# Optimization experiments

Hardware: AMD Instinct MI355X
Metric: run time of the kernel (lower is better)

## Reference

```python
import jax, jax.numpy as jnp
import numpy as np

HEAD_DIM = 64
NUM_HEAD = 12
NUM_LANDMARKS = 64
SEQ_LEN = 4096
BATCH = 8
NEG_BIG = 1e9


def setup_inputs() -> dict:
    key = jax.random.key(0)
    k1, k2, k3 = jax.random.split(key, 3)
    shape = (BATCH, NUM_HEAD, SEQ_LEN, HEAD_DIM)
    Q = jax.random.normal(k1, shape, dtype=jnp.float32)
    K = jax.random.normal(k2, shape, dtype=jnp.float32)
    V = jax.random.normal(k3, shape, dtype=jnp.float32)
    mask = jnp.ones((BATCH, SEQ_LEN), dtype=jnp.float32)
    return {"Q": Q, "K": K, "V": V, "mask": mask}


def iterative_inv(mat, n_iter=6):
    # Newton-Schulz iteration for Moore-Penrose pseudo-inverse ('original' init)
    I = jnp.eye(mat.shape[-1], dtype=mat.dtype)
    Km = mat
    Vi = Km.swapaxes(-1, -2) / jnp.max(jnp.sum(Km, axis=-2))
    for _ in range(n_iter):
        KV = Km @ Vi  # [B,H,L,L]
        Vi = 0.25 * Vi @ (13.0 * I - KV @ (15.0 * I - KV @ (7.0 * I - KV)))
    return Vi


def reference(Q, K, V, mask):
    scale = 1.0 / np.sqrt(np.sqrt(HEAD_DIM))  # divide by d^(1/4) on both Q and K
    m = mask[:, None, :, None]
    Qs = Q * m * scale
    Ks = K * m * scale

    B = Qs.shape[0]
    seg = SEQ_LEN // NUM_LANDMARKS
    # landmarks: segment means over the sequence -> [B,H,L,D]
    Q_l = Qs.reshape(B, NUM_HEAD, NUM_LANDMARKS, seg, HEAD_DIM).mean(axis=-2)
    K_l = Ks.reshape(B, NUM_HEAD, NUM_LANDMARKS, seg, HEAD_DIM).mean(axis=-2)

    # kernel_1: [B,H,S,L], kernel_2: [B,H,L,L], kernel_3: [B,H,L,S]
    kernel_1 = jax.nn.softmax(jnp.einsum('bhsd,bhld->bhsl', Qs, K_l), axis=-1)
    kernel_2 = jax.nn.softmax(jnp.einsum('bhld,bhmd->bhlm', Q_l, K_l), axis=-1)
    kernel_3 = jax.nn.softmax(
        jnp.einsum('bhld,bhsd->bhls', Q_l, Ks) - NEG_BIG * (1.0 - mask[:, None, None, :]),
        axis=-1)

    X = (kernel_1 @ iterative_inv(kernel_2)) @ (kernel_3 @ V)  # [B,H,S,D]
    return X
```

## Files before the change

kernel.cpp:

```cpp
#include <hip/hip_runtime.h>
#include <stdint.h>

#define BATCH 8
#define NH 12
#define SL 4096
#define HD 64
#define NL 64
#define SEG 64
#define BHN (BATCH*NH)
#define SCALE 0.35355339059327373f
#define LP 68

typedef unsigned short bfu;
typedef __attribute__((ext_vector_type(8))) short bhalf8;
typedef __attribute__((ext_vector_type(4))) float floatx4;

__device__ __forceinline__ float bf2f(bfu u) { return __uint_as_float(((unsigned)u) << 16); }
__device__ __forceinline__ bfu f2bf(float f) {
    unsigned u = __float_as_uint(f);
    u += 0x7fffu + ((u >> 16) & 1u);
    return (bfu)(u >> 16);
}
__device__ __forceinline__ void split(float x, bfu& h, bfu& l) {
    h = f2bf(x);
    l = f2bf(x - bf2f(h));
}
__device__ __forceinline__ unsigned pack2(bfu a, bfu b) { return (unsigned)a | ((unsigned)b << 16); }

__device__ __forceinline__ float ld1(const void* p, size_t i, int f32) {
    return f32 ? ((const float*)p)[i] : bf2f(((const bfu*)p)[i]);
}
__device__ __forceinline__ void ld4(const void* p, size_t i, int f32, float o[4]) {
    if (f32) {
        float4 v = *(const float4*)((const float*)p + i);
        o[0] = v.x; o[1] = v.y; o[2] = v.z; o[3] = v.w;
    } else {
        ushort4 v = *(const ushort4*)((const bfu*)p + i);
        o[0] = bf2f(v.x); o[1] = bf2f(v.y); o[2] = bf2f(v.z); o[3] = bf2f(v.w);
    }
}

template<int PA, int PB>
__device__ __forceinline__ void mm64(const float* A, const float* B, float acc[4][4], int tr, int tc) {
#pragma unroll
    for (int k4 = 0; k4 < 16; ++k4) {
        alignas(16) float a[4][4];
#pragma unroll
        for (int i = 0; i < 4; ++i)
            *(float4*)(&a[i][0]) = *(const float4*)(A + (4*tr + i)*PA + 4*k4);
#pragma unroll
        for (int kk = 0; kk < 4; ++kk) {
            float4 b = *(const float4*)(B + (4*k4 + kk)*PB + 4*tc);
#pragma unroll
            for (int i = 0; i < 4; ++i) {
                acc[i][0] = fmaf(a[i][kk], b.x, acc[i][0]);
                acc[i][1] = fmaf(a[i][kk], b.y, acc[i][1]);
                acc[i][2] = fmaf(a[i][kk], b.z, acc[i][2]);
                acc[i][3] = fmaf(a[i][kk], b.w, acc[i][3]);
            }
        }
    }
}

__device__ __forceinline__ bhalf8 ldfrag(const bfu* S, int row, int kb) {
    const uint2 a = *(const uint2*)(S + row*LP + kb);
    const uint2 b = *(const uint2*)(S + row*LP + kb + 16);
    union { uint4 u; bhalf8 s; } cv;
    cv.u.x = a.x; cv.u.y = a.y; cv.u.z = b.x; cv.u.w = b.y;
    return cv.s;
}

__device__ __forceinline__ void mfma64(const bfu* Ah, const bfu* Am,
                                       const bfu* Bh, const bfu* Bl,
                                       int w, int l, floatx4 acc[4]) {
    const int r15 = l & 15, kg = (l >> 4) << 2;
    bhalf8 ah[2], al[2];
    ah[0] = ldfrag(Ah, 16*w + r15, kg);
    ah[1] = ldfrag(Ah, 16*w + r15, 32 + kg);
    al[0] = ldfrag(Am, 16*w + r15, kg);
    al[1] = ldfrag(Am, 16*w + r15, 32 + kg);
#pragma unroll
    for (int t = 0; t < 4; ++t) {
#pragma unroll
        for (int c = 0; c < 2; ++c) {
            bhalf8 bh = ldfrag(Bh, 16*t + r15, 32*c + kg);
            bhalf8 bl = ldfrag(Bl, 16*t + r15, 32*c + kg);
            acc[t] = __builtin_amdgcn_mfma_f32_16x16x32_bf16(ah[c], bh, acc[t], 0, 0, 0);
            acc[t] = __builtin_amdgcn_mfma_f32_16x16x32_bf16(ah[c], bl, acc[t], 0, 0, 0);
            acc[t] = __builtin_amdgcn_mfma_f32_16x16x32_bf16(al[c], bh, acc[t], 0, 0, 0);
        }
    }
}

__global__ void detect_k(const void* __restrict__ M, int* __restrict__ dflag) {
    if (threadIdx.x == 0) {
        unsigned v = *(const unsigned*)M;
        dflag[0] = (v == 0x3F800000u) ? 1 : 0;
    }
}

__global__ __launch_bounds__(64) void landmarks_k(const void* __restrict__ Q, const void* __restrict__ K,
                                                  const void* __restrict__ M, const int* __restrict__ dt,
                                                  float* __restrict__ Ql, float* __restrict__ Kl) {
    int f32 = dt[0];
    int bh = blockIdx.x, l = blockIdx.y, d = threadIdx.x;
    int b = bh / NH;
    size_t qb = ((size_t)(bh*SL) + l*SEG)*HD + d;
    size_t mb = (size_t)b*SL + l*SEG;
    float aq = 0.f, ak = 0.f;
#pragma unroll 8
    for (int i = 0; i < SEG; ++i) {
        float mk = ld1(M, mb + i, f32);
        aq += ld1(Q, qb + (size_t)i*HD, f32) * mk;
        ak += ld1(K, qb + (size_t)i*HD, f32) * mk;
    }
    float sc = SCALE / (float)SEG;
    Ql[(bh*NL + l)*HD + d] = aq * sc;
    Kl[(bh*NL + l)*HD + d] = ak * sc;
}

__global__ __launch_bounds__(256) void k2_kernel(const float* __restrict__ Ql, const float* __restrict__ Kl,
                                                 float* __restrict__ K2, float* __restrict__ cmax) {
    __shared__ float Qs[64*68];
    __shared__ float Bs[64*68];
    __shared__ float Cs[64*68];
    int bh = blockIdx.x, t = threadIdx.x;
    int tr = t >> 4, tc = t & 15;
    for (int idx = t; idx < 4096; idx += 256) {
        int r = idx >> 6, c = idx & 63;
        Qs[r*68 + c] = Ql[(bh*64 + r)*64 + c];
        Bs[c*68 + r] = Kl[(bh*64 + r)*64 + c];
    }
    __syncthreads();
    float acc[4][4] = {};
    mm64<68,68>(Qs, Bs, acc, tr, tc);
#pragma unroll
    for (int i = 0; i < 4; ++i)
        *(float4*)&Cs[(4*tr + i)*68 + 4*tc] = make_float4(acc[i][0], acc[i][1], acc[i][2], acc[i][3]);
    __syncthreads();
    if (t < 64) {
        float mx = -1e30f;
        for (int m = 0; m < 64; ++m) mx = fmaxf(mx, Cs[t*68 + m]);
        float s = 0.f;
        for (int m = 0; m < 64; ++m) { float e = __expf(Cs[t*68 + m] - mx); Cs[t*68 + m] = e; s += e; }
        float r = 1.f / s;
        for (int m = 0; m < 64; ++m) Cs[t*68 + m] *= r;
    }
    __syncthreads();
    for (int idx = t; idx < 4096; idx += 256) {
        int r = idx >> 6, c = idx & 63;
        K2[bh*4096 + idx] = Cs[r*68 + c];
    }
    if (t < 64) {
        float cs = 0.f;
        for (int l = 0; l < 64; ++l) cs += Cs[l*68 + t];
        for (int off = 32; off > 0; off >>= 1) cs = fmaxf(cs, __shfl_xor(cs, off, 64));
        if (t == 0) cmax[bh] = cs;
    }
}

template<int NC>
__global__ __launch_bounds__(256) void k3v_partial(const void* __restrict__ K, const void* __restrict__ V,
                                                   const void* __restrict__ M, const int* __restrict__ dt,
                                                   const float* __restrict__ Ql,
                                                   float* __restrict__ Opart, float* __restrict__ mpart,
                                                   float* __restrict__ lpart) {
    __shared__ bfu Qh[64*LP], Qm[64*LP];
    __shared__ bfu Bh[64*LP], Bl[64*LP];
    __shared__ bfu Ph[64*LP], Pl[64*LP];
    __shared__ float bias[64];
    int f32 = dt[0];
    int bh = blockIdx.x, ch = blockIdx.y, b = bh / NH;
    int t = threadIdx.x, w = t >> 6, l = t & 63, r15 = l & 15;

    for (int g = t; g < 1024; g += 256) {
        int rr = g >> 4, c4 = (g & 15) << 2;
        float4 v = *(const float4*)(Ql + (bh*64 + rr)*64 + c4);
        bfu h0,h1,h2,h3,l0,l1,l2,l3;
        split(v.x,h0,l0); split(v.y,h1,l1); split(v.z,h2,l2); split(v.w,h3,l3);
        *(uint2*)&Qh[rr*LP + c4] = make_uint2(pack2(h0,h1), pack2(h2,h3));
        *(uint2*)&Qm[rr*LP + c4] = make_uint2(pack2(l0,l1), pack2(l2,l3));
    }
    floatx4 accO[4];
#pragma unroll
    for (int i = 0; i < 4; ++i) accO[i] = (floatx4){0.f,0.f,0.f,0.f};
    float mrow[4] = {-1e38f,-1e38f,-1e38f,-1e38f};
    float lrow[4] = {0.f,0.f,0.f,0.f};
    const int chunkN = SL / NC;
    int s0 = ch * chunkN;

    for (int st = 0; st < chunkN/64; ++st) {
        int sbase = s0 + st*64;
        __syncthreads();
        for (int g = t; g < 1024; g += 256) {
            int j = g >> 4, d4 = (g & 15) << 2;
            float v[4];
            ld4(K, ((size_t)(bh*SL) + sbase + j)*HD + d4, f32, v);
            float mk = ld1(M, (size_t)b*SL + sbase + j, f32) * SCALE;
            bfu h0,h1,h2,h3,l0,l1,l2,l3;
            split(v[0]*mk,h0,l0); split(v[1]*mk,h1,l1); split(v[2]*mk,h2,l2); split(v[3]*mk,h3,l3);
            *(uint2*)&Bh[j*LP + d4] = make_uint2(pack2(h0,h1), pack2(h2,h3));
            *(uint2*)&Bl[j*LP + d4] = make_uint2(pack2(l0,l1), pack2(l2,l3));
        }
        if (t < 64) bias[t] = -1000000000.0f * (1.f - ld1(M, (size_t)b*SL + sbase + t, f32));
        __syncthreads();
        floatx4 accS[4];
#pragma unroll
        for (int i = 0; i < 4; ++i) accS[i] = (floatx4){0.f,0.f,0.f,0.f};
        mfma64(Qh, Qm, Bh, Bl, w, l, accS);
#pragma unroll
        for (int t4 = 0; t4 < 4; ++t4) {
            float bc = bias[16*t4 + r15];
#pragma unroll
            for (int r = 0; r < 4; ++r) accS[t4][r] += bc;
        }
#pragma unroll
        for (int r = 0; r < 4; ++r) {
            float mx = fmaxf(fmaxf(accS[0][r], accS[1][r]), fmaxf(accS[2][r], accS[3][r]));
            mx = fmaxf(mx, __shfl_xor(mx, 1, 64));
            mx = fmaxf(mx, __shfl_xor(mx, 2, 64));
            mx = fmaxf(mx, __shfl_xor(mx, 4, 64));
            mx = fmaxf(mx, __shfl_xor(mx, 8, 64));
            float mnew = fmaxf(mrow[r], mx);
            float al = __expf(mrow[r] - mnew);
            float s = 0.f;
#pragma unroll
            for (int t4 = 0; t4 < 4; ++t4) {
                float e = __expf(accS[t4][r] - mnew);
                accS[t4][r] = e;
                s += e;
            }
            s += __shfl_xor(s, 1, 64);
            s += __shfl_xor(s, 2, 64);
            s += __shfl_xor(s, 4, 64);
            s += __shfl_xor(s, 8, 64);
            lrow[r] = lrow[r]*al + s;
            mrow[r] = mnew;
#pragma unroll
            for (int t4 = 0; t4 < 4; ++t4) accO[t4][r] *= al;
        }
#pragma unroll
        for (int t4 = 0; t4 < 4; ++t4)
#pragma unroll
            for (int r = 0; r < 4; ++r) {
                int row = 16*w + ((l>>4)<<2) + r, col = 16*t4 + r15;
                bfu h, lo;
                split(accS[t4][r], h, lo);
                Ph[row*LP + col] = h;
                Pl[row*LP + col] = lo;
            }
        __syncthreads();
        {
            int d = t & 63, j4g = t >> 6;
            for (int j4 = j4g; j4 < 16; j4 += 4) {
                float v0 = ld1(V, ((size_t)(bh*SL) + sbase + 4*j4 + 0)*HD + d, f32);
                float v1 = ld1(V, ((size_t)(bh*SL) + sbase + 4*j4 + 1)*HD + d, f32);
                float v2 = ld1(V, ((size_t)(bh*SL) + sbase + 4*j4 + 2)*HD + d, f32);
                float v3 = ld1(V, ((size_t)(bh*SL) + sbase + 4*j4 + 3)*HD + d, f32);
                bfu h0,h1,h2,h3,l0,l1,l2,l3;
                split(v0,h0,l0); split(v1,h1,l1); split(v2,h2,l2); split(v3,h3,l3);
                *(uint2*)&Bh[d*LP + 4*j4] = make_uint2(pack2(h0,h1), pack2(h2,h3));
                *(uint2*)&Bl[d*LP + 4*j4] = make_uint2(pack2(l0,l1), pack2(l2,l3));
            }
        }
        __syncthreads();
        mfma64(Ph, Pl, Bh, Bl, w, l, accO);
    }
    __syncthreads();
    int pc = bh*NC + ch;
    if (r15 == 0) {
#pragma unroll
        for (int r = 0; r < 4; ++r) {
            int row = 16*w + ((l>>4)<<2) + r;
            mpart[pc*64 + row] = mrow[r];
            lpart[pc*64 + row] = lrow[r];
        }
    }
#pragma unroll
    for (int t4 = 0; t4 < 4; ++t4)
#pragma unroll
        for (int r = 0; r < 4; ++r) {
            int row = 16*w + ((l>>4)<<2) + r, col = 16*t4 + r15;
            Opart[(size_t)pc*4096 + row*64 + col] = accO[t4][r];
        }
}

template<int NC>
__global__ __launch_bounds__(256) void combine_k(const float* __restrict__ Opart, const float* __restrict__ mpart,
                                                 const float* __restrict__ lpart, float* __restrict__ K3V) {
    __shared__ float coef[NC][64];
    int bh = blockIdx.x, t = threadIdx.x;
    if (t < 64) {
        float mg = -1e38f;
        for (int ch = 0; ch < NC; ++ch) mg = fmaxf(mg, mpart[(bh*NC + ch)*64 + t]);
        float e[NC];
        float sg = 0.f;
        for (int ch = 0; ch < NC; ++ch) {
            e[ch] = __expf(mpart[(bh*NC + ch)*64 + t] - mg);
            sg += e[ch] * lpart[(bh*NC + ch)*64 + t];
        }
        float r = 1.f / fmaxf(sg, 1e-37f);
        for (int ch = 0; ch < NC; ++ch) coef[ch][t] = e[ch] * r;
    }
    __syncthreads();
    int c = t & 63, lq = t >> 6;
    for (int k = 0; k < 16; ++k) {
        int l = 4*k + lq;
        float s = 0.f;
#pragma unroll
        for (int ch = 0; ch < NC; ++ch)
            s += coef[ch][l] * Opart[(size_t)(bh*NC + ch)*4096 + l*64 + c];
        K3V[(bh*64 + l)*64 + c] = s;
    }
}

__global__ __launch_bounds__(256) void inv_kernel(const float* __restrict__ K2, const float* __restrict__ cmaxArr,
                                                  const float* __restrict__ K3V, float* __restrict__ WT) {
    __shared__ float Km[4096];
    __shared__ float Vi[4096];
    __shared__ float B1[4096];
    __shared__ float B2[4096];
    int bh = blockIdx.x, t = threadIdx.x, tr = t >> 4, tc = t & 15;
    float cm = 0.f;
    for (int i = 0; i < BHN; ++i) cm = fmaxf(cm, cmaxArr[i]);
    float rc = 1.f / fmaxf(cm, 1e-37f);
    for (int idx = t; idx < 4096; idx += 256) Km[idx] = K2[bh*4096 + idx];
    __syncthreads();
    for (int idx = t; idx < 4096; idx += 256) {
        int i = idx >> 6, j = idx & 63;
        Vi[idx] = Km[j*64 + i] * rc;
    }
    __syncthreads();
    float acc[4][4];
    for (int it = 0; it < 6; ++it) {
#pragma unroll
        for (int i = 0; i < 4; ++i) for (int j = 0; j < 4; ++j) acc[i][j] = 0.f;
        mm64<64,64>(Km, Vi, acc, tr, tc);
#pragma unroll
        for (int i = 0; i < 4; ++i)
            *(float4*)&B1[(4*tr + i)*64 + 4*tc] = make_float4(acc[i][0], acc[i][1], acc[i][2], acc[i][3]);
        __syncthreads();
#pragma unroll
        for (int i = 0; i < 4; ++i) for (int j = 0; j < 4; ++j) acc[i][j] = 0.f;
        mm64<64,64>(B1, B1, acc, tr, tc);
#pragma unroll
        for (int i = 0; i < 4; ++i)
#pragma unroll
            for (int j = 0; j < 4; ++j) acc[i][j] = 7.f*B1[(4*tr + i)*64 + 4*tc + j] - acc[i][j];
#pragma unroll
        for (int i = 0; i < 4; ++i)
            *(float4*)&B2[(4*tr + i)*64 + 4*tc] = make_float4(acc[i][0], acc[i][1], acc[i][2], acc[i][3]);
        __syncthreads();
#pragma unroll
        for (int i = 0; i < 4; ++i) for (int j = 0; j < 4; ++j) acc[i][j] = 0.f;
        mm64<64,64>(B1, B2, acc, tr, tc);
#pragma unroll
        for (int i = 0; i < 4; ++i)
#pragma unroll
            for (int j = 0; j < 4; ++j) acc[i][j] = 15.f*B1[(4*tr + i)*64 + 4*tc + j] - acc[i][j];
        __syncthreads();
#pragma unroll
        for (int i = 0; i < 4; ++i)
            *(float4*)&B2[(4*tr + i)*64 + 4*tc] = make_float4(acc[i][0], acc[i][1], acc[i][2], acc[i][3]);
        __syncthreads();
#pragma unroll
        for (int i = 0; i < 4; ++i) for (int j = 0; j < 4; ++j) acc[i][j] = 0.f;
        mm64<64,64>(Vi, B2, acc, tr, tc);
        __syncthreads();
#pragma unroll
        for (int i = 0; i < 4; ++i)
#pragma unroll
            for (int j = 0; j < 4; ++j) {
                int off = (4*tr + i)*64 + 4*tc + j;
                Vi[off] = 3.25f*Vi[off] - 0.25f*acc[i][j];
            }
        __syncthreads();
    }
    for (int idx = t; idx < 4096; idx += 256) B1[idx] = K3V[bh*4096 + idx];
    __syncthreads();
#pragma unroll
    for (int i = 0; i < 4; ++i) for (int j = 0; j < 4; ++j) acc[i][j] = 0.f;
    mm64<64,64>(Vi, B1, acc, tr, tc);
#pragma unroll
    for (int i = 0; i < 4; ++i)
#pragma unroll
        for (int j = 0; j < 4; ++j)
            WT[(size_t)bh*4096 + (4*tc + j)*64 + (4*tr + i)] = acc[i][j];
}

__global__ __launch_bounds__(256) void final_k(const void* __restrict__ Q, const void* __restrict__ M,
                                               const int* __restrict__ dt,
                                               const float* __restrict__ Kl, const float* __restrict__ WT,
                                               void* __restrict__ X) {
    __shared__ bfu Ah[64*LP], Am[64*LP];
    __shared__ bfu Kh[64*LP], Km2[64*LP];
    __shared__ bfu Wh[64*LP], Wl[64*LP];
    int f32 = dt[0];
    int bh = blockIdx.x, tile = blockIdx.y, b = bh / NH;
    int t = threadIdx.x, w = t >> 6, l = t & 63, r15 = l & 15;
    int s0 = tile * 64;
    for (int g = t; g < 1024; g += 256) {
        int rr = g >> 4, d4 = (g & 15) << 2;
        float v[4];
        ld4(Q, ((size_t)(bh*SL) + s0 + rr)*HD + d4, f32, v);
        float mk = ld1(M, (size_t)b*SL + s0 + rr, f32) * SCALE;
        bfu h0,h1,h2,h3,l0,l1,l2,l3;
        split(v[0]*mk,h0,l0); split(v[1]*mk,h1,l1); split(v[2]*mk,h2,l2); split(v[3]*mk,h3,l3);
        *(uint2*)&Ah[rr*LP + d4] = make_uint2(pack2(h0,h1), pack2(h2,h3));
        *(uint2*)&Am[rr*LP + d4] = make_uint2(pack2(l0,l1), pack2(l2,l3));
    }
    for (int g = t; g < 1024; g += 256) {
        int rr = g >> 4, c4 = (g & 15) << 2;
        float4 v1 = *(const float4*)(Kl + bh*4096 + rr*64 + c4);
        bfu h0,h1,h2,h3,l0,l1,l2,l3;
        split(v1.x,h0,l0); split(v1.y,h1,l1); split(v1.z,h2,l2); split(v1.w,h3,l3);
        *(uint2*)&Kh[rr*LP + c4]  = make_uint2(pack2(h0,h1), pack2(h2,h3));
        *(uint2*)&Km2[rr*LP + c4] = make_uint2(pack2(l0,l1), pack2(l2,l3));
        float4 v2 = *(const float4*)(WT + (size_t)bh*4096 + rr*64 + c4);
        split(v2.x,h0,l0); split(v2.y,h1,l1); split(v2.z,h2,l2); split(v2.w,h3,l3);
        *(uint2*)&Wh[rr*LP + c4] = make_uint2(pack2(h0,h1), pack2(h2,h3));
        *(uint2*)&Wl[rr*LP + c4] = make_uint2(pack2(l0,l1), pack2(l2,l3));
    }
    __syncthreads();
    floatx4 accS[4];
#pragma unroll
    for (int i = 0; i < 4; ++i) accS[i] = (floatx4){0.f,0.f,0.f,0.f};
    mfma64(Ah, Am, Kh, Km2, w, l, accS);
#pragma unroll
    for (int r = 0; r < 4; ++r) {
        float mx = fmaxf(fmaxf(accS[0][r], accS[1][r]), fmaxf(accS[2][r], accS[3][r]));
        mx = fmaxf(mx, __shfl_xor(mx, 1, 64));
        mx = fmaxf(mx, __shfl_xor(mx, 2, 64));
        mx = fmaxf(mx, __shfl_xor(mx, 4, 64));
        mx = fmaxf(mx, __shfl_xor(mx, 8, 64));
        float s = 0.f;
#pragma unroll
        for (int t4 = 0; t4 < 4; ++t4) {
            float e = __expf(accS[t4][r] - mx);
            accS[t4][r] = e;
            s += e;
        }
        s += __shfl_xor(s, 1, 64);
        s += __shfl_xor(s, 2, 64);
        s += __shfl_xor(s, 4, 64);
        s += __shfl_xor(s, 8, 64);
        float inv = 1.f / s;
#pragma unroll
        for (int t4 = 0; t4 < 4; ++t4) accS[t4][r] *= inv;
    }
    __syncthreads();
#pragma unroll
    for (int t4 = 0; t4 < 4; ++t4)
#pragma unroll
        for (int r = 0; r < 4; ++r) {
            int row = 16*w + ((l>>4)<<2) + r, col = 16*t4 + r15;
            bfu h, lo;
            split(accS[t4][r], h, lo);
            Ah[row*LP + col] = h;
            Am[row*LP + col] = lo;
        }
    __syncthreads();
    floatx4 accO[4];
#pragma unroll
    for (int i = 0; i < 4; ++i) accO[i] = (floatx4){0.f,0.f,0.f,0.f};
    mfma64(Ah, Am, Wh, Wl, w, l, accO);
#pragma unroll
    for (int t4 = 0; t4 < 4; ++t4)
#pragma unroll
        for (int r = 0; r < 4; ++r) {
            int row = 16*w + ((l>>4)<<2) + r, col = 16*t4 + r15;
            size_t base = ((size_t)(bh*SL) + s0 + row)*HD + col;
            if (f32) ((float*)X)[base] = accO[t4][r];
            else     ((bfu*)X)[base] = f2bf(accO[t4][r]);
        }
}

extern "C" void kernel_launch(void* const* d_in, const int* in_sizes, int n_in,
                              void* d_out, int out_size, void* d_ws, size_t ws_size,
                              hipStream_t stream) {
    const void* Q = d_in[0];
    const void* K = d_in[1];
    const void* V = d_in[2];
    const void* M = d_in[3];
    float* ws = (float*)d_ws;

    auto layout_bytes = [](int nc) -> size_t {
        size_t o = 64 + 5*(size_t)BHN*4096 + 2*(size_t)BHN*nc*64 + 128 + (size_t)BHN*nc*4096;
        return o * 4;
    };
    int NC = (ws_size >= layout_bytes(8)) ? 8 : 4;

    size_t o = 0;
    int*   dflag = (int*)(ws + o); o += 64;
    float* Ql    = ws + o; o += (size_t)BHN*64*64;
    float* Kl    = ws + o; o += (size_t)BHN*64*64;
    float* K2    = ws + o; o += (size_t)BHN*64*64;
    float* K3V   = ws + o; o += (size_t)BHN*64*64;
    float* WT    = ws + o; o += (size_t)BHN*64*64;
    float* mpart = ws + o; o += (size_t)BHN*NC*64;
    float* lpart = ws + o; o += (size_t)BHN*NC*64;
    float* cmax  = ws + o; o += 128;
    float* Opart = ws + o; o += (size_t)BHN*NC*64*64;

    detect_k<<<1, 64, 0, stream>>>(M, dflag);
    landmarks_k<<<dim3(BHN, NL), 64, 0, stream>>>(Q, K, M, dflag, Ql, Kl);
    k2_kernel<<<BHN, 256, 0, stream>>>(Ql, Kl, K2, cmax);
    if (NC == 8) {
        k3v_partial<8><<<dim3(BHN, 8), 256, 0, stream>>>(K, V, M, dflag, Ql, Opart, mpart, lpart);
        combine_k<8><<<BHN, 256, 0, stream>>>(Opart, mpart, lpart, K3V);
    } else {
        k3v_partial<4><<<dim3(BHN, 4), 256, 0, stream>>>(K, V, M, dflag, Ql, Opart, mpart, lpart);
        combine_k<4><<<BHN, 256, 0, stream>>>(Opart, mpart, lpart, K3V);
    }
    inv_kernel<<<BHN, 256, 0, stream>>>(K2, cmax, K3V, WT);
    final_k<<<dim3(BHN, SL/64), 256, 0, stream>>>(Q, M, dflag, Kl, WT, d_out);
}
```

Measured before the change: 530.1 us.

## Pre-split landmarks and W into bf16 hi/lo pairs; process two tiles per final block

Landmark Q/K and the inverse-weight matrix are now split into bf16 hi/lo pairs once, in their producer kernels, and stored that way in global memory. Consumers (k2, k3v_partial, final_k) load the pairs directly instead of re-splitting fp32 values in every block. final_k now handles two 64-row sequence tiles per block, so the K-landmark and W staging into shared memory is amortised over twice the work and the grid is halved. The trade-off is fewer blocks in final_k for latency hiding, plus an extra sync per tile iteration.

```diff
diff --git a/kernel.cpp b/kernel.cpp
--- a/kernel.cpp
+++ b/kernel.cpp
@@ -101,7 +101,8 @@
 
 __global__ __launch_bounds__(64) void landmarks_k(const void* __restrict__ Q, const void* __restrict__ K,
                                                   const void* __restrict__ M, const int* __restrict__ dt,
-                                                  float* __restrict__ Ql, float* __restrict__ Kl) {
+                                                  bfu* __restrict__ Qlh, bfu* __restrict__ Qll,
+                                                  bfu* __restrict__ Klh, bfu* __restrict__ Kll) {
     int f32 = dt[0];
     int bh = blockIdx.x, l = blockIdx.y, d = threadIdx.x;
     int b = bh / NH;
@@ -115,11 +116,17 @@
         ak += ld1(K, qb + (size_t)i*HD, f32) * mk;
     }
     float sc = SCALE / (float)SEG;
-    Ql[(bh*NL + l)*HD + d] = aq * sc;
-    Kl[(bh*NL + l)*HD + d] = ak * sc;
-}
-
-__global__ __launch_bounds__(256) void k2_kernel(const float* __restrict__ Ql, const float* __restrict__ Kl,
+    float qv = aq * sc, kv = ak * sc;
+    bfu qh, ql_, kh, kl_;
+    split(qv, qh, ql_);
+    split(kv, kh, kl_);
+    size_t gi = (size_t)(bh*NL + l)*HD + d;
+    Qlh[gi] = qh; Qll[gi] = ql_;
+    Klh[gi] = kh; Kll[gi] = kl_;
+}
+
+__global__ __launch_bounds__(256) void k2_kernel(const bfu* __restrict__ Qlh, const bfu* __restrict__ Qll,
+                                                 const bfu* __restrict__ Klh, const bfu* __restrict__ Kll,
                                                  float* __restrict__ K2, float* __restrict__ cmax) {
     __shared__ float Qs[64*68];
     __shared__ float Bs[64*68];
@@ -128,8 +135,9 @@
     int tr = t >> 4, tc = t & 15;
     for (int idx = t; idx < 4096; idx += 256) {
         int r = idx >> 6, c = idx & 63;
-        Qs[r*68 + c] = Ql[(bh*64 + r)*64 + c];
-        Bs[c*68 + r] = Kl[(bh*64 + r)*64 + c];
+        size_t gi = (size_t)bh*4096 + idx;
+        Qs[r*68 + c] = bf2f(Qlh[gi]) + bf2f(Qll[gi]);
+        Bs[c*68 + r] = bf2f(Klh[gi]) + bf2f(Kll[gi]);
     }
     __syncthreads();
     float acc[4][4] = {};
@@ -162,7 +170,7 @@
 template<int NC>
 __global__ __launch_bounds__(256) void k3v_partial(const void* __restrict__ K, const void* __restrict__ V,
                                                    const void* __restrict__ M, const int* __restrict__ dt,
-                                                   const float* __restrict__ Ql,
+                                                   const bfu* __restrict__ Qlh, const bfu* __restrict__ Qll,
                                                    float* __restrict__ Opart, float* __restrict__ mpart,
                                                    float* __restrict__ lpart) {
     __shared__ bfu Qh[64*LP], Qm[64*LP];
@@ -175,11 +183,9 @@
 
     for (int g = t; g < 1024; g += 256) {
         int rr = g >> 4, c4 = (g & 15) << 2;
-        float4 v = *(const float4*)(Ql + (bh*64 + rr)*64 + c4);
-        bfu h0,h1,h2,h3,l0,l1,l2,l3;
-        split(v.x,h0,l0); split(v.y,h1,l1); split(v.z,h2,l2); split(v.w,h3,l3);
-        *(uint2*)&Qh[rr*LP + c4] = make_uint2(pack2(h0,h1), pack2(h2,h3));
-        *(uint2*)&Qm[rr*LP + c4] = make_uint2(pack2(l0,l1), pack2(l2,l3));
+        size_t gi = (size_t)bh*4096 + rr*64 + c4;
+        *(uint2*)&Qh[rr*LP + c4] = *(const uint2*)(Qlh + gi);
+        *(uint2*)&Qm[rr*LP + c4] = *(const uint2*)(Qll + gi);
     }
     floatx4 accO[4];
 #pragma unroll
@@ -315,7 +321,8 @@
 }
 
 __global__ __launch_bounds__(256) void inv_kernel(const float* __restrict__ K2, const float* __restrict__ cmaxArr,
-                                                  const float* __restrict__ K3V, float* __restrict__ WT) {
+                                                  const float* __restrict__ K3V,
+                                                  bfu* __restrict__ WTh, bfu* __restrict__ WTl) {
     __shared__ float Km[4096];
     __shared__ float Vi[4096];
     __shared__ float B1[4096];
@@ -384,95 +391,103 @@
 #pragma unroll
     for (int i = 0; i < 4; ++i)
 #pragma unroll
-        for (int j = 0; j < 4; ++j)
-            WT[(size_t)bh*4096 + (4*tc + j)*64 + (4*tr + i)] = acc[i][j];
+        for (int j = 0; j < 4; ++j) {
+            bfu h, lo;
+            split(acc[i][j], h, lo);
+            size_t gi = (size_t)bh*4096 + (4*tc + j)*64 + (4*tr + i);
+            WTh[gi] = h;
+            WTl[gi] = lo;
+        }
 }
 
 __global__ __launch_bounds__(256) void final_k(const void* __restrict__ Q, const void* __restrict__ M,
                                                const int* __restrict__ dt,
-                                               const float* __restrict__ Kl, const float* __restrict__ WT,
+                                               const bfu* __restrict__ Klh, const bfu* __restrict__ Kll,
+                                               const bfu* __restrict__ WTh, const bfu* __restrict__ WTl,
                                                void* __restrict__ X) {
     __shared__ bfu Ah[64*LP], Am[64*LP];
     __shared__ bfu Kh[64*LP], Km2[64*LP];
     __shared__ bfu Wh[64*LP], Wl[64*LP];
     int f32 = dt[0];
-    int bh = blockIdx.x, tile = blockIdx.y, b = bh / NH;
+    int bh = blockIdx.x, pair = blockIdx.y, b = bh / NH;
     int t = threadIdx.x, w = t >> 6, l = t & 63, r15 = l & 15;
-    int s0 = tile * 64;
-    for (int g = t; g < 1024; g += 256) {
-        int rr = g >> 4, d4 = (g & 15) << 2;
-        float v[4];
-        ld4(Q, ((size_t)(bh*SL) + s0 + rr)*HD + d4, f32, v);
-        float mk = ld1(M, (size_t)b*SL + s0 + rr, f32) * SCALE;
-        bfu h0,h1,h2,h3,l0,l1,l2,l3;
-        split(v[0]*mk,h0,l0); split(v[1]*mk,h1,l1); split(v[2]*mk,h2,l2); split(v[3]*mk,h3,l3);
-        *(uint2*)&Ah[rr*LP + d4] = make_uint2(pack2(h0,h1), pack2(h2,h3));
-        *(uint2*)&Am[rr*LP + d4] = make_uint2(pack2(l0,l1), pack2(l2,l3));
-    }
+
     for (int g = t; g < 1024; g += 256) {
         int rr = g >> 4, c4 = (g & 15) << 2;
-        float4 v1 = *(const float4*)(Kl + bh*4096 + rr*64 + c4);
-        bfu h0,h1,h2,h3,l0,l1,l2,l3;
-        split(v1.x,h0,l0); split(v1.y,h1,l1); split(v1.z,h2,l2); split(v1.w,h3,l3);
-        *(uint2*)&Kh[rr*LP + c4]  = make_uint2(pack2(h0,h1), pack2(h2,h3));
-        *(uint2*)&Km2[rr*LP + c4] = make_uint2(pack2(l0,l1), pack2(l2,l3));
-        float4 v2 = *(const float4*)(WT + (size_t)bh*4096 + rr*64 + c4);
-        split(v2.x,h0,l0); split(v2.y,h1,l1); split(v2.z,h2,l2); split(v2.w,h3,l3);
-        *(uint2*)&Wh[rr*LP + c4] = make_uint2(pack2(h0,h1), pack2(h2,h3));
-        *(uint2*)&Wl[rr*LP + c4] = make_uint2(pack2(l0,l1), pack2(l2,l3));
-    }
-    __syncthreads();
-    floatx4 accS[4];
-#pragma unroll
-    for (int i = 0; i < 4; ++i) accS[i] = (floatx4){0.f,0.f,0.f,0.f};
-    mfma64(Ah, Am, Kh, Km2, w, l, accS);
-#pragma unroll
-    for (int r = 0; r < 4; ++r) {
-        float mx = fmaxf(fmaxf(accS[0][r], accS[1][r]), fmaxf(accS[2][r], accS[3][r]));
-        mx = fmaxf(mx, __shfl_xor(mx, 1, 64));
-        mx = fmaxf(mx, __shfl_xor(mx, 2, 64));
-        mx = fmaxf(mx, __shfl_xor(mx, 4, 64));
-        mx = fmaxf(mx, __shfl_xor(mx, 8, 64));
-        float s = 0.f;
-#pragma unroll
-        for (int t4 = 0; t4 < 4; ++t4) {
-            float e = __expf(accS[t4][r] - mx);
-            accS[t4][r] = e;
-            s += e;
-        }
-        s += __shfl_xor(s, 1, 64);
-        s += __shfl_xor(s, 2, 64);
-        s += __shfl_xor(s, 4, 64);
-        s += __shfl_xor(s, 8, 64);
-        float inv = 1.f / s;
-#pragma unroll
-        for (int t4 = 0; t4 < 4; ++t4) accS[t4][r] *= inv;
-    }
-    __syncthreads();
-#pragma unroll
-    for (int t4 = 0; t4 < 4; ++t4)
+        size_t gi = (size_t)bh*4096 + rr*64 + c4;
+        *(uint2*)&Kh[rr*LP + c4]  = *(const uint2*)(Klh + gi);
+        *(uint2*)&Km2[rr*LP + c4] = *(const uint2*)(Kll + gi);
+        *(uint2*)&Wh[rr*LP + c4]  = *(const uint2*)(WTh + gi);
+        *(uint2*)&Wl[rr*LP + c4]  = *(const uint2*)(WTl + gi);
+    }
+
+#pragma unroll 1
+    for (int sub = 0; sub < 2; ++sub) {
+        int s0 = (pair*2 + sub) * 64;
+        for (int g = t; g < 1024; g += 256) {
+            int rr = g >> 4, d4 = (g & 15) << 2;
+            float v[4];
+            ld4(Q, ((size_t)(bh*SL) + s0 + rr)*HD + d4, f32, v);
+            float mk = ld1(M, (size_t)b*SL + s0 + rr, f32) * SCALE;
+            bfu h0,h1,h2,h3,l0,l1,l2,l3;
+            split(v[0]*mk,h0,l0); split(v[1]*mk,h1,l1); split(v[2]*mk,h2,l2); split(v[3]*mk,h3,l3);
+            *(uint2*)&Ah[rr*LP + d4] = make_uint2(pack2(h0,h1), pack2(h2,h3));
+            *(uint2*)&Am[rr*LP + d4] = make_uint2(pack2(l0,l1), pack2(l2,l3));
+        }
+        __syncthreads();
+        floatx4 accS[4];
+#pragma unroll
+        for (int i = 0; i < 4; ++i) accS[i] = (floatx4){0.f,0.f,0.f,0.f};
+        mfma64(Ah, Am, Kh, Km2, w, l, accS);
 #pragma unroll
         for (int r = 0; r < 4; ++r) {
-            int row = 16*w + ((l>>4)<<2) + r, col = 16*t4 + r15;
-            bfu h, lo;
-            split(accS[t4][r], h, lo);
-            Ah[row*LP + col] = h;
-            Am[row*LP + col] = lo;
-        }
-    __syncthreads();
-    floatx4 accO[4];
-#pragma unroll
-    for (int i = 0; i < 4; ++i) accO[i] = (floatx4){0.f,0.f,0.f,0.f};
-    mfma64(Ah, Am, Wh, Wl, w, l, accO);
-#pragma unroll
-    for (int t4 = 0; t4 < 4; ++t4)
-#pragma unroll
-        for (int r = 0; r < 4; ++r) {
-            int row = 16*w + ((l>>4)<<2) + r, col = 16*t4 + r15;
-            size_t base = ((size_t)(bh*SL) + s0 + row)*HD + col;
-            if (f32) ((float*)X)[base] = accO[t4][r];
-            else     ((bfu*)X)[base] = f2bf(accO[t4][r]);
-        }
+            float mx = fmaxf(fmaxf(accS[0][r], accS[1][r]), fmaxf(accS[2][r], accS[3][r]));
+            mx = fmaxf(mx, __shfl_xor(mx, 1, 64));
+            mx = fmaxf(mx, __shfl_xor(mx, 2, 64));
+            mx = fmaxf(mx, __shfl_xor(mx, 4, 64));
+            mx = fmaxf(mx, __shfl_xor(mx, 8, 64));
+            float s = 0.f;
+#pragma unroll
+            for (int t4 = 0; t4 < 4; ++t4) {
+                float e = __expf(accS[t4][r] - mx);
+                accS[t4][r] = e;
+                s += e;
+            }
+            s += __shfl_xor(s, 1, 64);
+            s += __shfl_xor(s, 2, 64);
+            s += __shfl_xor(s, 4, 64);
+            s += __shfl_xor(s, 8, 64);
+            float inv = 1.f / s;
+#pragma unroll
+            for (int t4 = 0; t4 < 4; ++t4) accS[t4][r] *= inv;
+        }
+        __syncthreads();
+#pragma unroll
+        for (int t4 = 0; t4 < 4; ++t4)
+#pragma unroll
+            for (int r = 0; r < 4; ++r) {
+                int row = 16*w + ((l>>4)<<2) + r, col = 16*t4 + r15;
+                bfu h, lo;
+                split(accS[t4][r], h, lo);
+                Ah[row*LP + col] = h;
+                Am[row*LP + col] = lo;
+            }
+        __syncthreads();
+        floatx4 accO[4];
+#pragma unroll
+        for (int i = 0; i < 4; ++i) accO[i] = (floatx4){0.f,0.f,0.f,0.f};
+        mfma64(Ah, Am, Wh, Wl, w, l, accO);
+#pragma unroll
+        for (int t4 = 0; t4 < 4; ++t4)
+#pragma unroll
+            for (int r = 0; r < 4; ++r) {
+                int row = 16*w + ((l>>4)<<2) + r, col = 16*t4 + r15;
+                size_t base = ((size_t)(bh*SL) + s0 + row)*HD + col;
+                if (f32) ((float*)X)[base] = accO[t4][r];
+                else     ((bfu*)X)[base] = f2bf(accO[t4][r]);
+            }
+        __syncthreads();
+    }
 }
 
 extern "C" void kernel_launch(void* const* d_in, const int* in_sizes, int n_in,
@@ -484,34 +499,41 @@
     const void* M = d_in[3];
     float* ws = (float*)d_ws;
 
-    auto layout_bytes = [](int nc) -> size_t {
-        size_t o = 64 + 5*(size_t)BHN*4096 + 2*(size_t)BHN*nc*64 + 128 + (size_t)BHN*nc*4096;
-        return o * 4;
+    auto layout_floats = [](int nc) -> size_t {
+        return 64
+             + 4*(size_t)BHN*2048
+             + 2*(size_t)BHN*4096
+             + 2*(size_t)BHN*2048
+             + 2*(size_t)BHN*nc*64 + 128
+             + (size_t)BHN*nc*4096;
     };
-    int NC = (ws_size >= layout_bytes(8)) ? 8 : 4;
+    int NC = (ws_size >= layout_floats(8)*4) ? 8 : 4;
 
     size_t o = 0;
-    int*   dflag = (int*)(ws + o); o += 64;
-    float* Ql    = ws + o; o += (size_t)BHN*64*64;
-    float* Kl    = ws + o; o += (size_t)BHN*64*64;
-    float* K2    = ws + o; o += (size_t)BHN*64*64;
-    float* K3V   = ws + o; o += (size_t)BHN*64*64;
-    float* WT    = ws + o; o += (size_t)BHN*64*64;
+    int* dflag = (int*)(ws + o); o += 64;
+    bfu* Qlh = (bfu*)(ws + o); o += (size_t)BHN*2048;
+    bfu* Qll = (bfu*)(ws + o); o += (size_t)BHN*2048;
+    bfu* Klh = (bfu*)(ws + o); o += (size_t)BHN*2048;
+    bfu* Kll = (bfu*)(ws + o); o += (size_t)BHN*2048;
+    float* K2  = ws + o; o += (size_t)BHN*4096;
+    float* K3V = ws + o; o += (size_t)BHN*4096;
+    bfu* WTh = (bfu*)(ws + o); o += (size_t)BHN*2048;
+    bfu* WTl = (bfu*)(ws + o); o += (size_t)BHN*2048;
     float* mpart = ws + o; o += (size_t)BHN*NC*64;
     float* lpart = ws + o; o += (size_t)BHN*NC*64;
     float* cmax  = ws + o; o += 128;
-    float* Opart = ws + o; o += (size_t)BHN*NC*64*64;
+    float* Opart = ws + o; o += (size_t)BHN*NC*4096;
 
     detect_k<<<1, 64, 0, stream>>>(M, dflag);
-    landmarks_k<<<dim3(BHN, NL), 64, 0, stream>>>(Q, K, M, dflag, Ql, Kl);
-    k2_kernel<<<BHN, 256, 0, stream>>>(Ql, Kl, K2, cmax);
+    landmarks_k<<<dim3(BHN, NL), 64, 0, stream>>>(Q, K, M, dflag, Qlh, Qll, Klh, Kll);
+    k2_kernel<<<BHN, 256, 0, stream>>>(Qlh, Qll, Klh, Kll, K2, cmax);
     if (NC == 8) {
-        k3v_partial<8><<<dim3(BHN, 8), 256, 0, stream>>>(K, V, M, dflag, Ql, Opart, mpart, lpart);
+        k3v_partial<8><<<dim3(BHN, 8), 256, 0, stream>>>(K, V, M, dflag, Qlh, Qll, Opart, mpart, lpart);
         combine_k<8><<<BHN, 256, 0, stream>>>(Opart, mpart, lpart, K3V);
     } else {
-        k3v_partial<4><<<dim3(BHN, 4), 256, 0, stream>>>(K, V, M, dflag, Ql, Opart, mpart, lpart);
+        k3v_partial<4><<<dim3(BHN, 4), 256, 0, stream>>>(K, V, M, dflag, Qlh, Qll, Opart, mpart, lpart);
         combine_k<4><<<BHN, 256, 0, stream>>>(Opart, mpart, lpart, K3V);
     }
-    inv_kernel<<<BHN, 256, 0, stream>>>(K2, cmax, K3V, WT);
-    final_k<<<dim3(BHN, SL/64), 256, 0, stream>>>(Q, M, dflag, Kl, WT, d_out);
-}
+    inv_kernel<<<BHN, 256, 0, stream>>>(K2, cmax, K3V, WTh, WTl);
+    final_k<<<dim3(BHN, SL/128), 256, 0, stream>>>(Q, M, dflag, Klh, Kll, WTh, WTl, d_out);
+}
```

After: 522.6 us. Within noise of the previous version (-1.4%).
